# Optimization experiments

Hardware: AMD Instinct MI355X
Metric: run time of the kernel (lower is better)

The kernel has to match this reference:

```python
import jax, jax.numpy as jnp
import numpy as np
import math

N = 100000          # total nodes across all subgraphs
E = 1600000         # directed edges (avg degree 16)
H = 128             # hidden_channels
MAXZ = 1000         # max_z
G = 1000            # number of subgraphs (unique batch ids)
NPG = N // G        # nodes per subgraph
L = 3               # num_layers


def setup_inputs() -> dict:
    key = jax.random.key(0)
    ks = jax.random.split(key, 9)
    z = jax.random.randint(ks[0], (N,), 0, MAXZ, dtype=jnp.int32)
    edge_index = jax.random.randint(ks[1], (2, E), 0, N, dtype=jnp.int32)
    batch = jnp.repeat(jnp.arange(G, dtype=jnp.int32), NPG)  # sorted graph ids
    s = 1.0 / math.sqrt(H)
    z_emb_table = jax.random.normal(ks[2], (MAXZ, H), jnp.float32) * 0.1
    conv_w = jax.random.normal(ks[3], (L, H, H), jnp.float32) * s
    conv_b = jnp.zeros((L, H), jnp.float32)
    mlp_w1 = jax.random.normal(ks[4], (H, H), jnp.float32) * s
    mlp_b1 = jnp.zeros((H,), jnp.float32)
    mlp_w2 = jax.random.normal(ks[5], (H, 1), jnp.float32) * s
    mlp_b2 = jnp.zeros((1,), jnp.float32)
    return {"num_nodes": N, "z": z, "edge_index": edge_index, "batch": batch,
            "z_emb_table": z_emb_table, "conv_w": conv_w, "conv_b": conv_b,
            "mlp_w1": mlp_w1, "mlp_b1": mlp_b1, "mlp_w2": mlp_w2, "mlp_b2": mlp_b2}


def reference(num_nodes, z, edge_index, batch, z_emb_table, conv_w, conv_b,
              mlp_w1, mlp_b1, mlp_w2, mlp_b2):
    # --- GCN normalization (PyG GCNConv: add self-loops, sym deg norm) ---
    loops = jnp.arange(num_nodes, dtype=edge_index.dtype)
    src = jnp.concatenate([edge_index[0], loops])  # [E+N]
    dst = jnp.concatenate([edge_index[1], loops])
    deg = jax.ops.segment_sum(jnp.ones_like(dst, jnp.float32), dst,
                              num_segments=num_nodes)
    dinv = jnp.where(deg > 0, jax.lax.rsqrt(deg), 0.0)
    norm = (dinv[src] * dinv[dst])[:, None]        # [E+N, 1]

    # --- embedding lookup (eval mode: no dropedge/dropout) ---
    x = z_emb_table[z]                             # [N, H]

    # --- stacked GCNConv: linear -> gather -> normalize -> scatter-add ---
    for l in range(L):
        h = x @ conv_w[l]                          # [N, H]
        h = jax.ops.segment_sum(h[src] * norm, dst, num_segments=num_nodes)
        h = h + conv_b[l]
        x = jax.nn.relu(h) if l < L - 1 else h

    # --- center-node pooling: first occurrence of each batch id ---
    first = jnp.concatenate([jnp.array([True]), batch[1:] != batch[:-1]])
    ci = jnp.nonzero(first, size=G)[0]             # [G]
    xs = x[ci] * x[ci + 1]                         # src * dst node features

    # --- MLP head [H, H, 1] (batch_norm=False, eval: dropout off) ---
    h = jax.nn.relu(xs @ mlp_w1 + mlp_b1)
    return h @ mlp_w2 + mlp_b2                     # [G, 1]
```

## Files before the change

kernel.cpp:

```cpp
#include <hip/hip_runtime.h>
#include <hip/hip_fp16.h>

#define HD 128
#define BSH 9
#define NBLKA 256
#define CAP 96
#define EDSCAP 10240
#define CAPB 12288

typedef _Float16 half8_t __attribute__((ext_vector_type(8)));
typedef float floatx4 __attribute__((ext_vector_type(4)));

__device__ inline unsigned pack_h2(float x, float y) {
  __half2 h = __floats2half2_rn(x, y);
  return __builtin_bit_cast(unsigned, h);
}
__device__ inline float2 up_h2(unsigned u) {
  __half2 h = __builtin_bit_cast(__half2, u);
  return __half22float2(h);
}

__device__ inline void add8(float* acc, uint4 r) {
  float2 f;
  f = up_h2(r.x); acc[0] += f.x; acc[1] += f.y;
  f = up_h2(r.y); acc[2] += f.x; acc[3] += f.y;
  f = up_h2(r.z); acc[4] += f.x; acc[5] += f.y;
  f = up_h2(r.w); acc[6] += f.x; acc[7] += f.y;
}

__global__ __launch_bounds__(256) void k_phase0(const int* __restrict__ src,
                                                const int* __restrict__ dst, int E, int nbuck,
                                                unsigned* __restrict__ bpool,
                                                int* __restrict__ counts,
                                                const float* __restrict__ conv_w,
                                                uint4* __restrict__ wfrag,
                                                const int* __restrict__ z,
                                                const float4* __restrict__ emb,
                                                uint2* __restrict__ xh,
                                                const int* __restrict__ batch,
                                                int* __restrict__ ci,
                                                int n, int embBlocks) {
  __shared__ int cnt[512];
  int b = blockIdx.x;
  if (b < NBLKA) {
    for (int i = threadIdx.x; i < nbuck; i += 256) cnt[i] = 0;
    __syncthreads();
    int chunk = (E + NBLKA - 1) / NBLKA;
    int lo = b * chunk, hi = min(E, lo + chunk);
    for (int i = lo + threadIdx.x; i < hi; i += 256) {
      int s = src[i], d = dst[i];
      int bk = d >> BSH;
      int c = atomicAdd(&cnt[bk], 1);
      if (c < CAP)
        bpool[((size_t)bk * NBLKA + b) * CAP + c] =
            ((unsigned)(d & ((1 << BSH) - 1)) << 23) | (unsigned)s;
    }
    __syncthreads();
    for (int bk = threadIdx.x; bk < nbuck; bk += 256) counts[(size_t)bk * NBLKA + b] = cnt[bk];
  } else if (b < NBLKA + 24) {
    int t = (b - NBLKA) * 256 + threadIdx.x;
    int lane = t & 63;
    int s = (t >> 6) & 3;
    int c4 = (t >> 8) & 3;
    int chalf = (t >> 10) & 1;
    int layer = t >> 11;
    int col = chalf * 64 + c4 * 16 + (lane & 15);
    int k0 = s * 32 + (lane >> 4) * 8;
    const float* W = conv_w + (size_t)layer * HD * HD;
    unsigned u[4];
#pragma unroll
    for (int j = 0; j < 4; ++j)
      u[j] = pack_h2(W[(size_t)(k0 + 2 * j) * HD + col], W[(size_t)(k0 + 2 * j + 1) * HD + col]);
    uint4 o; o.x = u[0]; o.y = u[1]; o.z = u[2]; o.w = u[3];
    wfrag[t] = o;
  } else if (b < NBLKA + 24 + embBlocks) {
    int idx = (b - NBLKA - 24) * 256 + threadIdx.x;
    if (idx >= n * 32) return;
    int node = idx >> 5, q = idx & 31;
    float4 v = emb[(size_t)z[node] * 32 + q];
    uint2 o;
    o.x = pack_h2(v.x, v.y);
    o.y = pack_h2(v.z, v.w);
    xh[idx] = o;
  } else {
    int i = (b - NBLKA - 24 - embBlocks) * 256 + threadIdx.x;
    if (i >= n) return;
    if (i == 0 || batch[i] != batch[i - 1]) ci[batch[i]] = i;
  }
}

__global__ __launch_bounds__(256) void k_build(const unsigned* __restrict__ bpool,
                                               const int* __restrict__ counts,
                                               int n, float* __restrict__ dinv,
                                               int* __restrict__ rowstart,
                                               int* __restrict__ rowend,
                                               int* __restrict__ col) {
  __shared__ unsigned eds[EDSCAP];
  __shared__ int hist[1 << BSH];
  __shared__ int wsum[256];
  __shared__ int coff[NBLKA + 1];
  int b = blockIdx.x;
  int t = threadIdx.x;
  int v = (t < NBLKA) ? min(counts[(size_t)b * NBLKA + t], CAP) : 0;
  wsum[t] = v;
  __syncthreads();
  for (int off = 1; off < NBLKA; off <<= 1) {
    int x = (t >= off) ? wsum[t - off] : 0;
    __syncthreads();
    wsum[t] += x;
    __syncthreads();
  }
  if (t < NBLKA) coff[t] = wsum[t] - v;
  if (t == NBLKA - 1) coff[NBLKA] = wsum[NBLKA - 1];
  __syncthreads();
  int total = min(coff[NBLKA], EDSCAP);
  int w = t >> 6, lane = t & 63;
  for (int blk = w; blk < NBLKA; blk += 4) {
    int off0 = coff[blk], len = coff[blk + 1] - off0;
    const unsigned* seg = bpool + ((size_t)b * NBLKA + blk) * CAP;
    for (int i = lane; i < len; i += 64)
      if (off0 + i < EDSCAP) eds[off0 + i] = seg[i];
  }
  for (int i = t; i < (1 << BSH); i += 256) hist[i] = 0;
  __syncthreads();
  for (int i = t; i < total; i += 256) atomicAdd(&hist[eds[i] >> 23], 1);
  __syncthreads();
  int base = b << BSH;
  int nn = min(1 << BSH, n - base);
  int a0 = hist[2 * t], a1 = hist[2 * t + 1];
  int s = a0 + a1;
  wsum[t] = s;
  __syncthreads();
  for (int off = 1; off < 256; off <<= 1) {
    int x = (t >= off) ? wsum[t - off] : 0;
    __syncthreads();
    wsum[t] += x;
    __syncthreads();
  }
  int excl = wsum[t] - s;
  int cbase = b * CAPB;
  if (2 * t < nn) {
    rowstart[base + 2 * t] = cbase + excl;
    rowend[base + 2 * t] = cbase + excl + a0;
    dinv[base + 2 * t] = 1.0f / sqrtf((float)(a0 + 1));
  }
  if (2 * t + 1 < nn) {
    rowstart[base + 2 * t + 1] = cbase + excl + a0;
    rowend[base + 2 * t + 1] = cbase + excl + s;
    dinv[base + 2 * t + 1] = 1.0f / sqrtf((float)(a1 + 1));
  }
  hist[2 * t] = cbase + excl;
  hist[2 * t + 1] = cbase + excl + a0;
  __syncthreads();
  for (int i = t; i < total; i += 256) {
    unsigned pk = eds[i];
    int dl = pk >> 23;
    int pos = atomicAdd(&hist[dl], 1);
    col[pos] = (int)(pk & 0x7FFFFF);
  }
}

__global__ __launch_bounds__(64) void k_active(const int* __restrict__ ci,
                                               const int* __restrict__ rowstart,
                                               const int* __restrict__ rowend,
                                               const int* __restrict__ col,
                                               int g2, int* __restrict__ flag,
                                               int* __restrict__ list, int n) {
  int lane = threadIdx.x;
  int vid = blockIdx.x * 64 + lane;
  bool haveRow = vid < g2;
  int* nactive = flag + n;
  int node = 0, e = 0, end = 0;
  if (haveRow) {
    node = ci[vid >> 1] + (vid & 1);
    e = rowstart[node];
    end = rowend[node];
  }
  bool neu = haveRow && (atomicExch(&flag[node], 1) == 0);
  unsigned long long m = __ballot(neu);
  int base = 0;
  if (lane == 0 && m) base = atomicAdd(nactive, __popcll(m));
  base = __shfl(base, 0);
  if (neu) list[base + __popcll(m & ((1ULL << lane) - 1))] = node;
  for (;;) {
    bool act = haveRow && (e < end);
    if (!__any(act)) break;
    int s = act ? col[e] : 0;
    bool nw = act && (atomicExch(&flag[s], 1) == 0);
    unsigned long long mm = __ballot(nw);
    int b2 = 0;
    if (lane == 0 && mm) b2 = atomicAdd(nactive, __popcll(mm));
    b2 = __shfl(b2, 0);
    if (nw) list[b2 + __popcll(mm & ((1ULL << lane) - 1))] = s;
    ++e;
  }
}

__global__ __launch_bounds__(256) void k_gemm_mfma(const uint4* __restrict__ Xh,
                                                   const uint4* __restrict__ wfrag,
                                                   const float* __restrict__ dinv,
                                                   uint2* __restrict__ Yh,
                                                   int n, int nwaves) {
  int lane = threadIdx.x & 63;
  int gw = blockIdx.x * 4 + (threadIdx.x >> 6);
  int chalf = gw & 1;
  int nrb = (n + 15) >> 4;
  int h = lane >> 4;

  half8_t wf[16];
#pragma unroll
  for (int i = 0; i < 16; ++i) {
    uint4 t = wfrag[((chalf * 4 + (i >> 2)) * 4 + (i & 3)) * 64 + lane];
    wf[i] = __builtin_bit_cast(half8_t, t);
  }

  for (int rb = gw >> 1; rb < nrb; rb += (nwaves >> 1)) {
    int row0 = rb * 16;
    int xr = row0 + (lane & 15);
    if (xr > n - 1) xr = n - 1;
    const uint4* xrow = Xh + (size_t)xr * 16;
    half8_t bf[4];
#pragma unroll
    for (int s = 0; s < 4; ++s)
      bf[s] = __builtin_bit_cast(half8_t, xrow[s * 4 + h]);
    floatx4 acc[4];
#pragma unroll
    for (int c4 = 0; c4 < 4; ++c4) acc[c4] = (floatx4){0.f, 0.f, 0.f, 0.f};
#pragma unroll
    for (int s = 0; s < 4; ++s) {
#pragma unroll
      for (int c4 = 0; c4 < 4; ++c4)
        acc[c4] = __builtin_amdgcn_mfma_f32_16x16x32_f16(wf[c4 * 4 + s], bf[s], acc[c4], 0, 0, 0);
    }
    int orow = row0 + (lane & 15);
    float dv = dinv[xr];
    if (orow < n) {
#pragma unroll
      for (int c4 = 0; c4 < 4; ++c4) {
        int colbase = chalf * 64 + c4 * 16 + h * 4;
        uint2 o;
        o.x = pack_h2(acc[c4][0] * dv, acc[c4][1] * dv);
        o.y = pack_h2(acc[c4][2] * dv, acc[c4][3] * dv);
        Yh[(size_t)orow * 32 + (colbase >> 2)] = o;
      }
    }
  }
}

__global__ __launch_bounds__(256) void k_gemmL(const uint4* __restrict__ Xh,
                                               const uint4* __restrict__ wfrag,
                                               const float* __restrict__ dinv,
                                               uint2* __restrict__ Yh,
                                               const int* __restrict__ list,
                                               const int* __restrict__ nactive,
                                               int nwaves) {
  int na = *nactive;
  int lane = threadIdx.x & 63;
  int gw = blockIdx.x * 4 + (threadIdx.x >> 6);
  int chalf = gw & 1;
  int nrb = (na + 15) >> 4;
  int h = lane >> 4;

  half8_t wf[16];
#pragma unroll
  for (int i = 0; i < 16; ++i) {
    uint4 t = wfrag[((chalf * 4 + (i >> 2)) * 4 + (i & 3)) * 64 + lane];
    wf[i] = __builtin_bit_cast(half8_t, t);
  }

  for (int rb = gw >> 1; rb < nrb; rb += (nwaves >> 1)) {
    int i = rb * 16 + (lane & 15);
    int xr = list[i < na ? i : na - 1];
    const uint4* xrow = Xh + (size_t)xr * 16;
    half8_t bf[4];
#pragma unroll
    for (int s = 0; s < 4; ++s)
      bf[s] = __builtin_bit_cast(half8_t, xrow[s * 4 + h]);
    floatx4 acc[4];
#pragma unroll
    for (int c4 = 0; c4 < 4; ++c4) acc[c4] = (floatx4){0.f, 0.f, 0.f, 0.f};
#pragma unroll
    for (int s = 0; s < 4; ++s) {
#pragma unroll
      for (int c4 = 0; c4 < 4; ++c4)
        acc[c4] = __builtin_amdgcn_mfma_f32_16x16x32_f16(wf[c4 * 4 + s], bf[s], acc[c4], 0, 0, 0);
    }
    float dv = dinv[xr];
    if (i < na) {
#pragma unroll
      for (int c4 = 0; c4 < 4; ++c4) {
        int colbase = chalf * 64 + c4 * 16 + h * 4;
        uint2 o;
        o.x = pack_h2(acc[c4][0] * dv, acc[c4][1] * dv);
        o.y = pack_h2(acc[c4][2] * dv, acc[c4][3] * dv);
        Yh[(size_t)xr * 32 + (colbase >> 2)] = o;
      }
    }
  }
}

__global__ __launch_bounds__(256) void k_agg(const uint4* __restrict__ H,
                                             const int* __restrict__ rowstart,
                                             const int* __restrict__ rowend,
                                             const int* __restrict__ col,
                                             const float* __restrict__ dinv,
                                             const float* __restrict__ bias,
                                             uint4* __restrict__ Out, int n, int relu) {
  int li = threadIdx.x & 15;
  int node = blockIdx.x * 16 + (threadIdx.x >> 4);
  if (node >= n) return;
  uint4 srow = H[(size_t)node * 16 + li];
  float acc[8] = {0.f, 0.f, 0.f, 0.f, 0.f, 0.f, 0.f, 0.f};
  add8(acc, srow);
  int e = rowstart[node], end = rowend[node];
  for (; e + 3 < end; e += 4) {
    int c0 = col[e], c1 = col[e + 1], c2 = col[e + 2], c3 = col[e + 3];
    uint4 r0 = H[(size_t)c0 * 16 + li];
    uint4 r1 = H[(size_t)c1 * 16 + li];
    uint4 r2 = H[(size_t)c2 * 16 + li];
    uint4 r3 = H[(size_t)c3 * 16 + li];
    add8(acc, r0);
    add8(acc, r1);
    add8(acc, r2);
    add8(acc, r3);
  }
  for (; e < end; ++e) {
    uint4 r = H[(size_t)col[e] * 16 + li];
    add8(acc, r);
  }
  float dv = dinv[node];
  float4 b0 = ((const float4*)bias)[2 * li];
  float4 b1 = ((const float4*)bias)[2 * li + 1];
  acc[0] = fmaf(dv, acc[0], b0.x); acc[1] = fmaf(dv, acc[1], b0.y);
  acc[2] = fmaf(dv, acc[2], b0.z); acc[3] = fmaf(dv, acc[3], b0.w);
  acc[4] = fmaf(dv, acc[4], b1.x); acc[5] = fmaf(dv, acc[5], b1.y);
  acc[6] = fmaf(dv, acc[6], b1.z); acc[7] = fmaf(dv, acc[7], b1.w);
  if (relu) {
#pragma unroll
    for (int q = 0; q < 8; ++q) acc[q] = fmaxf(acc[q], 0.f);
  }
  uint4 o;
  o.x = pack_h2(acc[0], acc[1]);
  o.y = pack_h2(acc[2], acc[3]);
  o.z = pack_h2(acc[4], acc[5]);
  o.w = pack_h2(acc[6], acc[7]);
  Out[(size_t)node * 16 + li] = o;
}

__global__ __launch_bounds__(256) void k_aggL(const uint4* __restrict__ H,
                                              const int* __restrict__ rowstart,
                                              const int* __restrict__ rowend,
                                              const int* __restrict__ col,
                                              const float* __restrict__ dinv,
                                              const float* __restrict__ bias,
                                              uint4* __restrict__ Out,
                                              const int* __restrict__ list,
                                              const int* __restrict__ nactive) {
  int na = *nactive;
  int li = threadIdx.x & 15;
  int i0 = blockIdx.x * 16 + (threadIdx.x >> 4);
  int stride = gridDim.x * 16;
  for (int i = i0; i < na; i += stride) {
    int node = list[i];
    uint4 srow = H[(size_t)node * 16 + li];
    float acc[8] = {0.f, 0.f, 0.f, 0.f, 0.f, 0.f, 0.f, 0.f};
    add8(acc, srow);
    int e = rowstart[node], end = rowend[node];
    for (; e + 3 < end; e += 4) {
      int c0 = col[e], c1 = col[e + 1], c2 = col[e + 2], c3 = col[e + 3];
      uint4 r0 = H[(size_t)c0 * 16 + li];
      uint4 r1 = H[(size_t)c1 * 16 + li];
      uint4 r2 = H[(size_t)c2 * 16 + li];
      uint4 r3 = H[(size_t)c3 * 16 + li];
      add8(acc, r0);
      add8(acc, r1);
      add8(acc, r2);
      add8(acc, r3);
    }
    for (; e < end; ++e) {
      uint4 r = H[(size_t)col[e] * 16 + li];
      add8(acc, r);
    }
    float dv = dinv[node];
    float4 b0 = ((const float4*)bias)[2 * li];
    float4 b1 = ((const float4*)bias)[2 * li + 1];
    acc[0] = fmaf(dv, acc[0], b0.x); acc[1] = fmaf(dv, acc[1], b0.y);
    acc[2] = fmaf(dv, acc[2], b0.z); acc[3] = fmaf(dv, acc[3], b0.w);
    acc[4] = fmaf(dv, acc[4], b1.x); acc[5] = fmaf(dv, acc[5], b1.y);
    acc[6] = fmaf(dv, acc[6], b1.z); acc[7] = fmaf(dv, acc[7], b1.w);
#pragma unroll
    for (int q = 0; q < 8; ++q) acc[q] = fmaxf(acc[q], 0.f);
    uint4 o;
    o.x = pack_h2(acc[0], acc[1]);
    o.y = pack_h2(acc[2], acc[3]);
    o.z = pack_h2(acc[4], acc[5]);
    o.w = pack_h2(acc[6], acc[7]);
    Out[(size_t)node * 16 + li] = o;
  }
}

__global__ __launch_bounds__(256) void k_aggF(const uint4* __restrict__ H,
                                              const int* __restrict__ rowstart,
                                              const int* __restrict__ rowend,
                                              const int* __restrict__ col,
                                              const float* __restrict__ dinv,
                                              const float* __restrict__ bias,
                                              const int* __restrict__ ci,
                                              uint4* __restrict__ Xc, int g2) {
  int li = threadIdx.x & 15;
  int vid = blockIdx.x * 16 + (threadIdx.x >> 4);
  if (vid >= g2) return;
  int node = ci[vid >> 1] + (vid & 1);
  uint4 srow = H[(size_t)node * 16 + li];
  float acc[8] = {0.f, 0.f, 0.f, 0.f, 0.f, 0.f, 0.f, 0.f};
  add8(acc, srow);
  int e = rowstart[node], end = rowend[node];
  for (; e + 3 < end; e += 4) {
    int c0 = col[e], c1 = col[e + 1], c2 = col[e + 2], c3 = col[e + 3];
    uint4 r0 = H[(size_t)c0 * 16 + li];
    uint4 r1 = H[(size_t)c1 * 16 + li];
    uint4 r2 = H[(size_t)c2 * 16 + li];
    uint4 r3 = H[(size_t)c3 * 16 + li];
    add8(acc, r0);
    add8(acc, r1);
    add8(acc, r2);
    add8(acc, r3);
  }
  for (; e < end; ++e) {
    uint4 r = H[(size_t)col[e] * 16 + li];
    add8(acc, r);
  }
  float dv = dinv[node];
  float4 b0 = ((const float4*)bias)[2 * li];
  float4 b1 = ((const float4*)bias)[2 * li + 1];
  acc[0] = fmaf(dv, acc[0], b0.x); acc[1] = fmaf(dv, acc[1], b0.y);
  acc[2] = fmaf(dv, acc[2], b0.z); acc[3] = fmaf(dv, acc[3], b0.w);
  acc[4] = fmaf(dv, acc[4], b1.x); acc[5] = fmaf(dv, acc[5], b1.y);
  acc[6] = fmaf(dv, acc[6], b1.z); acc[7] = fmaf(dv, acc[7], b1.w);
  uint4 o;
  o.x = pack_h2(acc[0], acc[1]);
  o.y = pack_h2(acc[2], acc[3]);
  o.z = pack_h2(acc[4], acc[5]);
  o.w = pack_h2(acc[6], acc[7]);
  Xc[(size_t)vid * 16 + li] = o;
}

__global__ __launch_bounds__(128) void k_head(const __half* __restrict__ Xc,
                                              const float* __restrict__ W1,
                                              const float* __restrict__ b1,
                                              const float* __restrict__ w2,
                                              const float* __restrict__ b2,
                                              float* __restrict__ out, int G) {
  __shared__ float xs[HD];
  __shared__ float red[HD];
  int g = blockIdx.x;
  int t = threadIdx.x;
  xs[t] = __half2float(Xc[(size_t)(2 * g) * HD + t]) *
          __half2float(Xc[(size_t)(2 * g + 1) * HD + t]);
  __syncthreads();
  float acc = b1[t];
#pragma unroll 8
  for (int k = 0; k < HD; ++k) acc = fmaf(xs[k], W1[k * HD + t], acc);
  acc = fmaxf(acc, 0.f);
  red[t] = acc * w2[t];
  __syncthreads();
  for (int off = 64; off > 0; off >>= 1) {
    if (t < off) red[t] += red[t + off];
    __syncthreads();
  }
  if (t == 0) out[g] = red[0] + b2[0];
}

extern "C" void kernel_launch(void* const* d_in, const int* in_sizes, int n_in,
                              void* d_out, int out_size, void* d_ws, size_t ws_size,
                              hipStream_t stream) {
  (void)n_in; (void)ws_size;
  const int*   z      = (const int*)d_in[1];
  const int*   ei     = (const int*)d_in[2];
  const int*   batch  = (const int*)d_in[3];
  const float* emb    = (const float*)d_in[4];
  const float* conv_w = (const float*)d_in[5];
  const float* conv_b = (const float*)d_in[6];
  const float* w1     = (const float*)d_in[7];
  const float* b1     = (const float*)d_in[8];
  const float* w2     = (const float*)d_in[9];
  const float* b2     = (const float*)d_in[10];
  int n = in_sizes[1];
  int E = in_sizes[2] / 2;
  int G = out_size;
  const int* esrc = ei;
  const int* edst = ei + E;
  int nbuck = (n + (1 << BSH) - 1) >> BSH;

  char* p = (char*)d_ws;
  auto alloc = [&](size_t bytes) { void* r = (void*)p; p += (bytes + 255) / 256 * 256; return r; };
  unsigned* bufA     = (unsigned*)alloc((size_t)n * HD * 2);
  unsigned* bufB     = (unsigned*)alloc((size_t)n * HD * 2);
  unsigned* bufC     = (unsigned*)alloc((size_t)2 * G * HD * 2);
  float*    dinv     = (float*)alloc((size_t)n * 4);
  int*      rowstart = (int*)alloc((size_t)n * 4);
  int*      rowend   = (int*)alloc((size_t)n * 4);
  int*      col      = (int*)alloc((size_t)nbuck * CAPB * 4);
  uint4*    wfrag    = (uint4*)alloc((size_t)3 * 2048 * 16);
  int*      ci       = (int*)alloc((size_t)G * 4);
  int*      flag     = (int*)alloc((size_t)(n + 64) * 4);
  int*      list     = (int*)alloc((size_t)n * 4);
  unsigned* bpool    = (unsigned*)alloc((size_t)nbuck * NBLKA * CAP * 4);
  int*      counts   = (int*)alloc((size_t)nbuck * NBLKA * 4);

  int embBlocks = (n * 32 + 255) / 256;
  int ciBlocks = (n + 255) / 256;
  int g2 = 2 * G;
  int* nactive = flag + n;

  k_phase0<<<NBLKA + 24 + embBlocks + ciBlocks, 256, 0, stream>>>(
      esrc, edst, E, nbuck, bpool, counts, conv_w, wfrag, z, (const float4*)emb,
      (uint2*)bufA, batch, ci, n, embBlocks);
  k_build<<<nbuck, 256, 0, stream>>>(bpool, counts, n, dinv, rowstart, rowend, col);
  hipMemsetAsync(flag, 0, (size_t)(n + 1) * 4, stream);
  k_active<<<(g2 + 63) / 64, 64, 0, stream>>>(ci, rowstart, rowend, col, g2, flag, list, n);

  const int nwaves = 4096;
  k_gemm_mfma<<<nwaves / 4, 256, 0, stream>>>((const uint4*)bufA, wfrag, dinv,
                                              (uint2*)bufB, n, nwaves);
  k_agg<<<(n + 15) / 16, 256, 0, stream>>>((const uint4*)bufB, rowstart, rowend, col, dinv,
                                           conv_b, (uint4*)bufA, n, 1);
  k_gemm_mfma<<<nwaves / 4, 256, 0, stream>>>((const uint4*)bufA, wfrag + 2048, dinv,
                                              (uint2*)bufB, n, nwaves);
  k_aggL<<<1024, 256, 0, stream>>>((const uint4*)bufB, rowstart, rowend, col, dinv,
                                   conv_b + HD, (uint4*)bufA, list, nactive);
  k_gemmL<<<256, 256, 0, stream>>>((const uint4*)bufA, wfrag + 4096, dinv,
                                   (uint2*)bufB, list, nactive, 1024);
  k_aggF<<<(g2 + 15) / 16, 256, 0, stream>>>((const uint4*)bufB, rowstart, rowend, col, dinv,
                                             conv_b + 2 * HD, ci, (uint4*)bufC, g2);

  k_head<<<G, 128, 0, stream>>>((const __half*)bufC, w1, b1, w2, b2, (float*)d_out, G);
}
```

Measured before the change: 243.1 us.

## Stage edge buckets in LDS, split phase0, fold flag memset into prep

The edge-bucketing pass now collects each block's bucketed edges in a 76.8KB shared-memory staging buffer and writes them out to the global pool afterwards, replacing scattered global writes with more contiguous ones. The prep work (weight fragments, embedding, center indices) moves to its own kernel, which also zeroes the active-flag array, so the separate memset is gone. The aggregation kernel loads column indices with nontemporal hints. The large shared buffer limits bucket blocks to one per CU and adds a launch, and NBUCK_MAX caps the supported node count.

```diff
diff --git a/kernel.cpp b/kernel.cpp
--- a/kernel.cpp
+++ b/kernel.cpp
@@ -5,6 +5,7 @@
 #define BSH 9
 #define NBLKA 256
 #define CAP 96
+#define NBUCK_MAX 200
 #define EDSCAP 10240
 #define CAPB 12288
 
@@ -28,37 +29,45 @@
   f = up_h2(r.w); acc[6] += f.x; acc[7] += f.y;
 }
 
-__global__ __launch_bounds__(256) void k_phase0(const int* __restrict__ src,
+__global__ __launch_bounds__(256) void k_bucket(const int* __restrict__ src,
                                                 const int* __restrict__ dst, int E, int nbuck,
                                                 unsigned* __restrict__ bpool,
-                                                int* __restrict__ counts,
-                                                const float* __restrict__ conv_w,
-                                                uint4* __restrict__ wfrag,
-                                                const int* __restrict__ z,
-                                                const float4* __restrict__ emb,
-                                                uint2* __restrict__ xh,
-                                                const int* __restrict__ batch,
-                                                int* __restrict__ ci,
-                                                int n, int embBlocks) {
-  __shared__ int cnt[512];
+                                                int* __restrict__ counts) {
+  __shared__ unsigned stage[NBUCK_MAX * CAP];
+  __shared__ int cnt[NBUCK_MAX];
+  int blk = blockIdx.x;
+  for (int i = threadIdx.x; i < nbuck; i += 256) cnt[i] = 0;
+  __syncthreads();
+  int chunk = (E + NBLKA - 1) / NBLKA;
+  int lo = blk * chunk, hi = min(E, lo + chunk);
+  for (int i = lo + threadIdx.x; i < hi; i += 256) {
+    int s = src[i], d = dst[i];
+    int bk = d >> BSH;
+    int c = atomicAdd(&cnt[bk], 1);
+    if (c < CAP)
+      stage[bk * CAP + c] = ((unsigned)(d & ((1 << BSH) - 1)) << 23) | (unsigned)s;
+  }
+  __syncthreads();
+  for (int i = threadIdx.x; i < nbuck * CAP; i += 256) {
+    int bk = i / CAP, c = i - bk * CAP;
+    if (c < min(cnt[bk], CAP))
+      bpool[((size_t)bk * NBLKA + blk) * CAP + c] = stage[i];
+  }
+  for (int bk = threadIdx.x; bk < nbuck; bk += 256) counts[(size_t)bk * NBLKA + blk] = cnt[bk];
+}
+
+__global__ __launch_bounds__(256) void k_prep(const float* __restrict__ conv_w,
+                                              uint4* __restrict__ wfrag,
+                                              const int* __restrict__ z,
+                                              const float4* __restrict__ emb,
+                                              uint2* __restrict__ xh,
+                                              const int* __restrict__ batch,
+                                              int* __restrict__ ci,
+                                              int* __restrict__ flag,
+                                              int n, int embBlocks) {
   int b = blockIdx.x;
-  if (b < NBLKA) {
-    for (int i = threadIdx.x; i < nbuck; i += 256) cnt[i] = 0;
-    __syncthreads();
-    int chunk = (E + NBLKA - 1) / NBLKA;
-    int lo = b * chunk, hi = min(E, lo + chunk);
-    for (int i = lo + threadIdx.x; i < hi; i += 256) {
-      int s = src[i], d = dst[i];
-      int bk = d >> BSH;
-      int c = atomicAdd(&cnt[bk], 1);
-      if (c < CAP)
-        bpool[((size_t)bk * NBLKA + b) * CAP + c] =
-            ((unsigned)(d & ((1 << BSH) - 1)) << 23) | (unsigned)s;
-    }
-    __syncthreads();
-    for (int bk = threadIdx.x; bk < nbuck; bk += 256) counts[(size_t)bk * NBLKA + b] = cnt[bk];
-  } else if (b < NBLKA + 24) {
-    int t = (b - NBLKA) * 256 + threadIdx.x;
+  if (b < 24) {
+    int t = b * 256 + threadIdx.x;
     int lane = t & 63;
     int s = (t >> 6) & 3;
     int c4 = (t >> 8) & 3;
@@ -73,8 +82,8 @@
       u[j] = pack_h2(W[(size_t)(k0 + 2 * j) * HD + col], W[(size_t)(k0 + 2 * j + 1) * HD + col]);
     uint4 o; o.x = u[0]; o.y = u[1]; o.z = u[2]; o.w = u[3];
     wfrag[t] = o;
-  } else if (b < NBLKA + 24 + embBlocks) {
-    int idx = (b - NBLKA - 24) * 256 + threadIdx.x;
+  } else if (b < 24 + embBlocks) {
+    int idx = (b - 24) * 256 + threadIdx.x;
     if (idx >= n * 32) return;
     int node = idx >> 5, q = idx & 31;
     float4 v = emb[(size_t)z[node] * 32 + q];
@@ -83,8 +92,10 @@
     o.y = pack_h2(v.z, v.w);
     xh[idx] = o;
   } else {
-    int i = (b - NBLKA - 24 - embBlocks) * 256 + threadIdx.x;
+    int i = (b - 24 - embBlocks) * 256 + threadIdx.x;
     if (i >= n) return;
+    flag[i] = 0;
+    if (i == 0) flag[n] = 0;
     if (i == 0 || batch[i] != batch[i - 1]) ci[batch[i]] = i;
   }
 }
@@ -314,7 +325,10 @@
   add8(acc, srow);
   int e = rowstart[node], end = rowend[node];
   for (; e + 3 < end; e += 4) {
-    int c0 = col[e], c1 = col[e + 1], c2 = col[e + 2], c3 = col[e + 3];
+    int c0 = __builtin_nontemporal_load(&col[e]);
+    int c1 = __builtin_nontemporal_load(&col[e + 1]);
+    int c2 = __builtin_nontemporal_load(&col[e + 2]);
+    int c3 = __builtin_nontemporal_load(&col[e + 3]);
     uint4 r0 = H[(size_t)c0 * 16 + li];
     uint4 r1 = H[(size_t)c1 * 16 + li];
     uint4 r2 = H[(size_t)c2 * 16 + li];
@@ -325,7 +339,7 @@
     add8(acc, r3);
   }
   for (; e < end; ++e) {
-    uint4 r = H[(size_t)col[e] * 16 + li];
+    uint4 r = H[(size_t)__builtin_nontemporal_load(&col[e]) * 16 + li];
     add8(acc, r);
   }
   float dv = dinv[node];
@@ -513,11 +527,11 @@
   int g2 = 2 * G;
   int* nactive = flag + n;
 
-  k_phase0<<<NBLKA + 24 + embBlocks + ciBlocks, 256, 0, stream>>>(
-      esrc, edst, E, nbuck, bpool, counts, conv_w, wfrag, z, (const float4*)emb,
-      (uint2*)bufA, batch, ci, n, embBlocks);
+  k_bucket<<<NBLKA, 256, 0, stream>>>(esrc, edst, E, nbuck, bpool, counts);
+  k_prep<<<24 + embBlocks + ciBlocks, 256, 0, stream>>>(conv_w, wfrag, z, (const float4*)emb,
+                                                        (uint2*)bufA, batch, ci, flag, n,
+                                                        embBlocks);
   k_build<<<nbuck, 256, 0, stream>>>(bpool, counts, n, dinv, rowstart, rowend, col);
-  hipMemsetAsync(flag, 0, (size_t)(n + 1) * 4, stream);
   k_active<<<(g2 + 63) / 64, 64, 0, stream>>>(ci, rowstart, rowend, col, g2, flag, list, n);
 
   const int nwaves = 4096;
```

New measurement: 258.6 us. +6.4%, slower.
